# Optimization experiments

Measured on AMD Instinct MI355X. Metric: run time of the kernel, lower is better.

## Reference

```python
import jax, jax.numpy as jnp
import numpy as np

N = 4096
IN_F = 128
OUT_F = 64      # per-head out_features
HEADS = 4
ALPHA = 0.2     # LeakyReLU negative slope
NEG_FILL = -9e15


def setup_inputs() -> dict:
    key = jax.random.key(0)
    k_h, k_adj, k_W, k_a = jax.random.split(key, 4)
    h = jax.random.normal(k_h, (N, IN_F), dtype=jnp.float32)
    adj = jax.random.randint(k_adj, (N, N), 0, 2, dtype=jnp.int32)
    W = jax.random.normal(k_W, (IN_F, OUT_F * HEADS), dtype=jnp.float32) * 0.1
    a = jax.random.normal(k_a, (2 * OUT_F, 1), dtype=jnp.float32) * 0.1
    bias = jnp.zeros((OUT_F * HEADS,), dtype=jnp.float32)
    return {"h": h, "adj": adj, "W": W, "a": a, "bias": bias}


def reference(h, adj, W, a, bias):
    n = h.shape[0]
    Wh = (h @ W).reshape(n, HEADS, OUT_F)            # (N, H, F)
    # e_ij = leakyrelu(a_left . Wh_i + a_right . Wh_j)  (decomposed outer sum;
    # same math as concat([Wh_i, Wh_j]) @ a in the original)
    a_left = a[:OUT_F, 0]                            # (F,)
    a_right = a[OUT_F:, 0]                           # (F,)
    left = jnp.einsum('nhf,f->nh', Wh, a_left)       # (N, H)
    right = jnp.einsum('nhf,f->nh', Wh, a_right)     # (N, H)
    mask = adj > 0                                   # (N, N)
    outs = []
    for head in range(HEADS):                        # small fixed loop over heads
        e = left[:, head, None] + right[None, :, head]          # (N, N)
        e = jnp.where(e >= 0, e, ALPHA * e)                      # LeakyReLU
        e = jnp.where(mask, e, NEG_FILL)
        attn = jax.nn.softmax(e, axis=1)                         # (N, N)
        outs.append(attn @ Wh[:, head, :])                       # (N, F)
    out = jnp.concatenate(outs, axis=1)              # concat=True -> (N, H*F)
    return out + bias
```

## Files before the change

### kernel.cpp

```cpp
#include <hip/hip_runtime.h>
#include <hip/hip_bf16.h>

#define NN 4096
#define IN_F 128
#define OUT_F 64
#define C_TOT 256
#define ALPHA 0.2f
#define LOG2E 1.4426950408889634f

typedef float f32x4 __attribute__((ext_vector_type(4)));
typedef float f32x2 __attribute__((ext_vector_type(2)));
typedef __bf16 bf16x8 __attribute__((ext_vector_type(8)));

__device__ __forceinline__ unsigned fmap(float f) {
    unsigned u = __float_as_uint(f);
    return (u >> 31) ? ~u : (u | 0x80000000u);
}
__device__ __forceinline__ float funmap(unsigned u) {
    return (u >> 31) ? __uint_as_float(u & 0x7FFFFFFFu) : __uint_as_float(~u);
}
__device__ __forceinline__ unsigned short bfbits(float x) {
    union { __bf16 b; unsigned short u; } t;
    t.b = (__bf16)x;
    return t.u;
}
__device__ __forceinline__ void gl16(const void* g, void* l) {
    __builtin_amdgcn_global_load_lds((const __attribute__((address_space(1))) void*)g,
                                     (__attribute__((address_space(3))) void*)l, 16, 0, 0);
}

__global__ __launch_bounds__(256) void k_mask(
    const int* __restrict__ adj, unsigned* __restrict__ mask,
    const float* __restrict__ W, const float* __restrict__ a,
    unsigned short* __restrict__ WTbf, float* __restrict__ uLR,
    unsigned int* __restrict__ Rmax)
{
    const int tid = threadIdx.x;
    const int lane = tid & 63, wv = tid >> 6;
    const int row = blockIdx.x * 4 + wv;
    const int* __restrict__ ar = adj + (size_t)row * NN;
    unsigned* __restrict__ mr = mask + (size_t)row * 128;
    for (int c = 0; c < 8; ++c) {
        const int j0 = c * 512;
        unsigned w = 0u;
#pragma unroll
        for (int k = 0; k < 8; ++k) {
            const unsigned long long bb = __ballot(ar[j0 + k * 64 + lane] > 0);
            const unsigned lo = (unsigned)bb, hi = (unsigned)(bb >> 32);
            if ((lane >> 1) == k) w = (lane & 1) ? hi : lo;
        }
        if (lane < 16) {
            const int wi = c * 16 + lane;
            mr[(wi & 3) * 32 + (wi >> 2)] = w;
        }
    }

    if (blockIdx.x < 32) {
        const int b = blockIdx.x;
        const int c = b * 8 + (tid & 7);
#pragma unroll
        for (int pass = 0; pass < 4; ++pass) {
            const int k = pass * 32 + (tid >> 3);
            WTbf[(size_t)c * IN_F + k] = bfbits(W[k * C_TOT + c]);
        }
        if (b == 0) {
            if (tid < 4) Rmax[tid] = 0u;
            for (int o = tid; o < 1024; o += 256) {
                const int k = o >> 3, j = o & 7;
                const int hd = j & 3, side = j >> 2;
                float s = 0.f;
                for (int f = 0; f < OUT_F; ++f)
                    s = fmaf(W[k * C_TOT + hd * OUT_F + f], a[side * OUT_F + f], s);
                uLR[k * 8 + side * 4 + hd] = s;
            }
        }
    }
}

__global__ __launch_bounds__(256) void k_prep(
    const float* __restrict__ hmat, const unsigned short* __restrict__ WTbf,
    const float* __restrict__ uLR, unsigned short* __restrict__ WhT,
    float* __restrict__ leftT, float* __restrict__ rightT,
    unsigned int* __restrict__ Rmax)
{
    __shared__ float hs[16][132];
    __shared__ float us[128][8];
    const int tid = threadIdx.x;
    const int rowbase = blockIdx.x * 16;

    ((float4*)us)[tid] = ((const float4*)uLR)[tid];
#pragma unroll
    for (int p = 0; p < 8; ++p) {
        const int idx = p * 256 + tid;
        hs[idx >> 7][idx & 127] = hmat[(size_t)rowbase * IN_F + idx];
    }
    __syncthreads();

    const int lane = tid & 63, wv = tid >> 6;
    const int m16 = lane & 15, kg = lane >> 4;

    if (wv == 0) {
        const int row = lane >> 2, hd = lane & 3;
        float aL = 0.f, aR = 0.f;
#pragma unroll
        for (int k = 0; k < 128; k += 4) {
            const float4 hv = *(const float4*)&hs[row][k];
            aL = fmaf(hv.x, us[k][hd],   fmaf(hv.y, us[k+1][hd],   fmaf(hv.z, us[k+2][hd],   fmaf(hv.w, us[k+3][hd],   aL))));
            aR = fmaf(hv.x, us[k][hd+4], fmaf(hv.y, us[k+1][hd+4], fmaf(hv.z, us[k+2][hd+4], fmaf(hv.w, us[k+3][hd+4], aR))));
        }
        leftT [hd * NN + rowbase + row] = aL;
        rightT[hd * NN + rowbase + row] = aR * LOG2E;
        float mx = aR;
#pragma unroll
        for (int s = 4; s < 64; s <<= 1) mx = fmaxf(mx, __shfl_xor(mx, s, 64));
        if (lane < 4) atomicMax(&Rmax[hd], fmap(mx));
    }

    bf16x8 afr[4];
#pragma unroll
    for (int ks = 0; ks < 4; ++ks) {
        const float4 lo = *(const float4*)&hs[m16][ks * 32 + kg * 8];
        const float4 hi = *(const float4*)&hs[m16][ks * 32 + kg * 8 + 4];
        bf16x8 v;
        v[0] = (__bf16)lo.x; v[1] = (__bf16)lo.y; v[2] = (__bf16)lo.z; v[3] = (__bf16)lo.w;
        v[4] = (__bf16)hi.x; v[5] = (__bf16)hi.y; v[6] = (__bf16)hi.z; v[7] = (__bf16)hi.w;
        afr[ks] = v;
    }

#pragma unroll
    for (int nt0 = 0; nt0 < 4; ++nt0) {
        const int col = (wv * 4 + nt0) * 16 + m16;
        f32x4 acc = (f32x4){0.f, 0.f, 0.f, 0.f};
#pragma unroll
        for (int ks = 0; ks < 4; ++ks) {
            union { uint4 u; bf16x8 v; } B;
            B.u = *(const uint4*)(WTbf + (size_t)col * IN_F + ks * 32 + kg * 8);
            acc = __builtin_amdgcn_mfma_f32_16x16x32_bf16(afr[ks], B.v, acc, 0, 0, 0);
        }
#pragma unroll
        for (int i = 0; i < 4; ++i)
            WhT[(size_t)col * NN + rowbase + kg * 4 + i] = bfbits(acc[i]);
    }
}

__global__ __launch_bounds__(512, 8) void k_attn(
    const unsigned* __restrict__ mask,
    const unsigned short* __restrict__ WhT,
    const float* __restrict__ leftT,
    const float* __restrict__ rightT,
    const unsigned int* __restrict__ Rmax,
    float* __restrict__ out,
    float* __restrict__ num1,
    float* __restrict__ den)
{
    __shared__ unsigned short Bb[2][64 * 128];
    __shared__ float rlds[2048];

    const int tid = threadIdx.x;
    const int lane = tid & 63;
    const int wv = tid >> 6;
    const int rh = wv & 1;
    const int j4 = wv >> 1;
    const int jh = blockIdx.x & 1;
    const int hd = (blockIdx.x >> 1) & 3;
    const int rowbase = (blockIdx.x >> 3) * 32;
    const int m = lane & 15;
    const int kg = lane >> 4;
    const int sh = kg * 8;

    *(float4*)&rlds[tid * 4] =
        *(const float4*)(rightT + (size_t)hd * NN + jh * 2048 + tid * 4);
    unsigned mreg[16];
    {
        const unsigned* mrow = mask + (size_t)(rowbase + rh * 16 + m) * 128
                               + j4 * 32 + jh * 16;
#pragma unroll
        for (int p = 0; p < 4; ++p) {
            const uint4 v = *(const uint4*)(mrow + p * 4);
            mreg[p * 4 + 0] = v.x; mreg[p * 4 + 1] = v.y;
            mreg[p * 4 + 2] = v.z; mreg[p * 4 + 3] = v.w;
        }
    }

    const float lf = leftT[hd * NN + rowbase + rh * 16 + m];
    const float rmx = funmap(Rmax[hd]);
    const float x = lf + rmx;
    const float m0v = fmaxf(x, ALPHA * x);
    const float mp0 = m0v * LOG2E;
    const float lf2 = fmaf(lf, LOG2E, -mp0);
    const float qc = -0.8f * mp0;
    const f32x2 lf22 = (f32x2){lf2, lf2};
    const f32x2 al2  = (f32x2){ALPHA, ALPHA};
    const f32x2 qc2  = (f32x2){qc, qc};

    bf16x8 ONE8;
#pragma unroll
    for (int i = 0; i < 8; ++i) ONE8[i] = (__bf16)1.0f;

    const int srow0 = wv * 4 + (lane >> 4);
    const int g_lin = lane & 15;
    const int lg = g_lin ^ (srow0 & 15);
    const unsigned short* gsrc0 = WhT + (size_t)(hd * 64 + srow0) * NN
                                  + jh * 2048 + lg * 8;
    const unsigned short* gsrc1 = gsrc0 + (size_t)32 * NN;
    const int d0 = wv * 512 + lane * 8;

#define STAGE(buf, t) {                                  \
    gl16(gsrc0 + (t) * 128, &Bb[buf][d0]);               \
    gl16(gsrc1 + (t) * 128, &Bb[buf][4096 + d0]); }

    const int pg8 = ((j4 * 4 + kg) ^ m) * 8;
    const int bro = m * 128 + pg8;

    f32x4 acc0 = (f32x4){0,0,0,0}, acc1 = acc0, acc2 = acc0, acc3 = acc0;
    f32x4 accL = (f32x4){0,0,0,0};

    union F4 { f32x4 v; f32x2 h[2]; };

#define COMPUTE(buf, t) {                                                        \
    const unsigned aw = mreg[(t)] >> sh;                                         \
    F4 RA, RB;                                                                   \
    RA.v = *(const f32x4*)&rlds[(t) * 128 + j4 * 32 + sh];                       \
    RB.v = *(const f32x4*)&rlds[(t) * 128 + j4 * 32 + sh + 4];                   \
    const f32x2 rp2[4] = { RA.h[0], RA.h[1], RB.h[0], RB.h[1] };                 \
    union { __bf16 b[8]; bf16x8 v; } Af;                                         \
    _Pragma("unroll")                                                            \
    for (int e = 0; e < 4; ++e) {                                                \
        const f32x2 p = rp2[e] + lf22;                                           \
        const f32x2 q = __builtin_elementwise_fma(p, al2, qc2);                  \
        const float t0 = fmaxf(p.x, q.x), t1 = fmaxf(p.y, q.y);                  \
        float w0 = exp2f(t0), w1 = exp2f(t1);                                    \
        const unsigned mk0 = (unsigned)(((int)(aw << (31 - 2*e)))     >> 31);    \
        const unsigned mk1 = (unsigned)(((int)(aw << (31 - (2*e+1)))) >> 31);    \
        w0 = __uint_as_float(__float_as_uint(w0) & mk0);                         \
        w1 = __uint_as_float(__float_as_uint(w1) & mk1);                         \
        Af.b[2*e]   = (__bf16)w0;                                                \
        Af.b[2*e+1] = (__bf16)w1;                                                \
    }                                                                            \
    union { uint4 u; bf16x8 v; } B0, B1, B2, B3;                                 \
    B0.u = *(const uint4*)&Bb[buf][bro];                                         \
    B1.u = *(const uint4*)&Bb[buf][bro + 2048];                                  \
    B2.u = *(const uint4*)&Bb[buf][bro + 4096];                                  \
    B3.u = *(const uint4*)&Bb[buf][bro + 6144];                                  \
    acc0 = __builtin_amdgcn_mfma_f32_16x16x32_bf16(Af.v, B0.v, acc0, 0, 0, 0);   \
    acc1 = __builtin_amdgcn_mfma_f32_16x16x32_bf16(Af.v, B1.v, acc1, 0, 0, 0);   \
    acc2 = __builtin_amdgcn_mfma_f32_16x16x32_bf16(Af.v, B2.v, acc2, 0, 0, 0);   \
    acc3 = __builtin_amdgcn_mfma_f32_16x16x32_bf16(Af.v, B3.v, acc3, 0, 0, 0);   \
    accL = __builtin_amdgcn_mfma_f32_16x16x32_bf16(Af.v, ONE8, accL, 0, 0, 0);   \
}

    STAGE(0, 0);
    __syncthreads();

#pragma unroll
    for (int t = 0; t < 16; ++t) {
        if (t + 1 < 16) {
            STAGE((t + 1) & 1, t + 1);
            asm volatile("s_waitcnt vmcnt(2)" ::: "memory");
        } else {
            asm volatile("s_waitcnt vmcnt(0)" ::: "memory");
        }
        __builtin_amdgcn_sched_barrier(0);
        COMPUTE(t & 1, t);
        __builtin_amdgcn_sched_barrier(0);
        __builtin_amdgcn_s_barrier();
    }
#undef STAGE
#undef COMPUTE

    __syncthreads();
    float* comb = (float*)&Bb[0][0];
    if (j4 > 0) {
        float* c = comb + (((j4 - 1) * 2 + rh) * 64 + lane) * 20;
#pragma unroll
        for (int i = 0; i < 4; ++i) {
            c[ 0 + i] = acc0[i]; c[ 4 + i] = acc1[i];
            c[ 8 + i] = acc2[i]; c[12 + i] = acc3[i];
            c[16 + i] = accL[i];
        }
    }
    __syncthreads();
    if (j4 == 0) {
#pragma unroll
        for (int pt = 0; pt < 3; ++pt) {
            const float* c = comb + ((pt * 2 + rh) * 64 + lane) * 20;
#pragma unroll
            for (int i = 0; i < 4; ++i) {
                acc0[i] += c[ 0 + i]; acc1[i] += c[ 4 + i];
                acc2[i] += c[ 8 + i]; acc3[i] += c[12 + i];
                accL[i] += c[16 + i];
            }
        }
        float* numdst = jh ? num1 : out;
#pragma unroll
        for (int q = 0; q < 4; ++q) {
            const f32x4 A = (q == 0) ? acc0 : (q == 1) ? acc1 : (q == 2) ? acc2 : acc3;
            const int col = hd * 64 + q * 16 + m;
#pragma unroll
            for (int i = 0; i < 4; ++i) {
                const int r = kg * 4 + i;
                numdst[(size_t)(rowbase + rh * 16 + r) * C_TOT + col] = A[i];
            }
        }
        if (m == 0) {
#pragma unroll
            for (int i = 0; i < 4; ++i)
                den[(size_t)jh * 4 * NN + hd * NN + rowbase + rh * 16 + kg * 4 + i] = accL[i];
        }
    }
}

__global__ __launch_bounds__(256) void k_fin(
    float* __restrict__ out, const float* __restrict__ num1,
    const float* __restrict__ den, const float* __restrict__ bias)
{
    const int idx = blockIdx.x * 256 + threadIdx.x;
    const int row = idx >> 6;
    const int c4 = (idx & 63) * 4;
    const int hd = c4 >> 6;
    const float d = den[hd * NN + row] + den[4 * NN + hd * NN + row];
    const float rd = 1.0f / d;
    float4 n0 = *(float4*)(out + (size_t)row * C_TOT + c4);
    const float4 n1 = *(const float4*)(num1 + (size_t)row * C_TOT + c4);
    const float4 bv = *(const float4*)(bias + c4);
    n0.x = fmaf(n0.x + n1.x, rd, bv.x);
    n0.y = fmaf(n0.y + n1.y, rd, bv.y);
    n0.z = fmaf(n0.z + n1.z, rd, bv.z);
    n0.w = fmaf(n0.w + n1.w, rd, bv.w);
    *(float4*)(out + (size_t)row * C_TOT + c4) = n0;
}

extern "C" void kernel_launch(void* const* d_in, const int* in_sizes, int n_in,
                              void* d_out, int out_size, void* d_ws, size_t ws_size,
                              hipStream_t stream) {
    const float* hmat = (const float*)d_in[0];
    const int*   adj  = (const int*)d_in[1];
    const float* W    = (const float*)d_in[2];
    const float* a    = (const float*)d_in[3];
    const float* bias = (const float*)d_in[4];
    float* out = (float*)d_out;

    char* ws = (char*)d_ws;
    unsigned short* WhT  = (unsigned short*)(ws + 0x000000);
    float* rightT        = (float*)(ws + 0x280000);
    float* leftT         = (float*)(ws + 0x2A0000);
    unsigned short* WTbf = (unsigned short*)(ws + 0x2B0000);
    float* uLR           = (float*)(ws + 0x2C0000);
    unsigned int* Rmax   = (unsigned int*)(ws + 0x2C1000);
    unsigned* mask       = (unsigned*)(ws + 0x300000);
    float* num1          = (float*)(ws + 0x500000);
    float* den           = (float*)(ws + 0x900000);

    hipLaunchKernelGGL(k_mask, dim3(1024), dim3(256), 0, stream,
                       adj, mask, W, a, WTbf, uLR, Rmax);
    hipLaunchKernelGGL(k_prep, dim3(256),  dim3(256), 0, stream,
                       hmat, WTbf, uLR, WhT, leftT, rightT, Rmax);
    hipLaunchKernelGGL(k_attn, dim3(1024), dim3(512), 0, stream,
                       mask, WhT, leftT, rightT, Rmax, out, num1, den);
    hipLaunchKernelGGL(k_fin,  dim3(1024), dim3(256), 0, stream,
                       out, num1, den, bias);
}
```

Baseline: 71.34 us.

## Factor exp of leaky scores, enlarge attention blocks, deepen B staging pipeline

Rewrites the per-element weight exp2(max(p, alpha*p+c)) as max(exp(l)*exp(r), exp(alpha*l)*exp(alpha*r)). The exponentials of the right-hand terms are precomputed once per block in LDS and the per-row factors are computed once per thread, so the inner loop drops its transcendental ops in favour of multiplies. Blocks grow to 1024 threads covering 64 rows, which halves the grid and doubles reuse of each staged B tile. The B tile ring goes from 2 to 4 buffers with 3 tiles in flight, and the barrier now sits before the next stage. Risks are overflow or underflow in the factored products, higher LDS use, and lower occupancy at 1024 threads.

```diff
diff --git a/kernel.cpp b/kernel.cpp
--- a/kernel.cpp
+++ b/kernel.cpp
@@ -143,7 +143,7 @@
     }
 }
 
-__global__ __launch_bounds__(512, 8) void k_attn(
+__global__ __launch_bounds__(1024, 8) void k_attn(
     const unsigned* __restrict__ mask,
     const unsigned short* __restrict__ WhT,
     const float* __restrict__ leftT,
@@ -153,23 +153,41 @@
     float* __restrict__ num1,
     float* __restrict__ den)
 {
-    __shared__ unsigned short Bb[2][64 * 128];
-    __shared__ float rlds[2048];
+    __shared__ unsigned short Bb[4][64 * 128];
+    __shared__ float erl[2048];
+    __shared__ float er2l[2048];
 
     const int tid = threadIdx.x;
     const int lane = tid & 63;
-    const int wv = tid >> 6;
-    const int rh = wv & 1;
-    const int j4 = wv >> 1;
+    const int wvi = tid >> 6;
+    const int rh = wvi & 3;
+    const int j4 = wvi >> 2;
     const int jh = blockIdx.x & 1;
     const int hd = (blockIdx.x >> 1) & 3;
-    const int rowbase = (blockIdx.x >> 3) * 32;
+    const int rowbase = (blockIdx.x >> 3) * 64;
     const int m = lane & 15;
     const int kg = lane >> 4;
     const int sh = kg * 8;
 
-    *(float4*)&rlds[tid * 4] =
-        *(const float4*)(rightT + (size_t)hd * NN + jh * 2048 + tid * 4);
+    const int srow = tid >> 4;
+    const int g_lin = tid & 15;
+    const int lg = g_lin ^ (srow & 15);
+    const unsigned short* gsrc = WhT + (size_t)(hd * 64 + srow) * NN
+                                 + jh * 2048 + lg * 8;
+    const int d0 = srow * 128 + g_lin * 8;
+
+#define STAGE(buf, t) { gl16(gsrc + (t) * 128, &Bb[buf][d0]); }
+
+    STAGE(0, 0); STAGE(1, 1); STAGE(2, 2);
+
+    {
+        const float2 rv = *(const float2*)(rightT + (size_t)hd * NN + jh * 2048 + tid * 2);
+        erl [tid * 2    ] = exp2f(rv.x);
+        erl [tid * 2 + 1] = exp2f(rv.y);
+        er2l[tid * 2    ] = exp2f(ALPHA * rv.x);
+        er2l[tid * 2 + 1] = exp2f(ALPHA * rv.y);
+    }
+
     unsigned mreg[16];
     {
         const unsigned* mrow = mask + (size_t)(rowbase + rh * 16 + m) * 128
@@ -187,27 +205,16 @@
     const float x = lf + rmx;
     const float m0v = fmaxf(x, ALPHA * x);
     const float mp0 = m0v * LOG2E;
-    const float lf2 = fmaf(lf, LOG2E, -mp0);
-    const float qc = -0.8f * mp0;
-    const f32x2 lf22 = (f32x2){lf2, lf2};
-    const f32x2 al2  = (f32x2){ALPHA, ALPHA};
-    const f32x2 qc2  = (f32x2){qc, qc};
+    const float EL  = exp2f(fmaf(lf,         LOG2E, -mp0));
+    const float EL2 = exp2f(fmaf(lf * ALPHA, LOG2E, -mp0));
+    const f32x2 ELv  = (f32x2){EL,  EL};
+    const f32x2 EL2v = (f32x2){EL2, EL2};
 
     bf16x8 ONE8;
 #pragma unroll
     for (int i = 0; i < 8; ++i) ONE8[i] = (__bf16)1.0f;
 
-    const int srow0 = wv * 4 + (lane >> 4);
-    const int g_lin = lane & 15;
-    const int lg = g_lin ^ (srow0 & 15);
-    const unsigned short* gsrc0 = WhT + (size_t)(hd * 64 + srow0) * NN
-                                  + jh * 2048 + lg * 8;
-    const unsigned short* gsrc1 = gsrc0 + (size_t)32 * NN;
-    const int d0 = wv * 512 + lane * 8;
-
-#define STAGE(buf, t) {                                  \
-    gl16(gsrc0 + (t) * 128, &Bb[buf][d0]);               \
-    gl16(gsrc1 + (t) * 128, &Bb[buf][4096 + d0]); }
+    __syncthreads();
 
     const int pg8 = ((j4 * 4 + kg) ^ m) * 8;
     const int bro = m * 128 + pg8;
@@ -219,17 +226,20 @@
 
 #define COMPUTE(buf, t) {                                                        \
     const unsigned aw = mreg[(t)] >> sh;                                         \
-    F4 RA, RB;                                                                   \
-    RA.v = *(const f32x4*)&rlds[(t) * 128 + j4 * 32 + sh];                       \
-    RB.v = *(const f32x4*)&rlds[(t) * 128 + j4 * 32 + sh + 4];                   \
-    const f32x2 rp2[4] = { RA.h[0], RA.h[1], RB.h[0], RB.h[1] };                 \
+    F4 E0, E1, F0, F1;                                                           \
+    E0.v = *(const f32x4*)&erl [(t) * 128 + j4 * 32 + sh];                       \
+    E1.v = *(const f32x4*)&erl [(t) * 128 + j4 * 32 + sh + 4];                   \
+    F0.v = *(const f32x4*)&er2l[(t) * 128 + j4 * 32 + sh];                       \
+    F1.v = *(const f32x4*)&er2l[(t) * 128 + j4 * 32 + sh + 4];                   \
+    const f32x2 ep[4] = { E0.h[0], E0.h[1], E1.h[0], E1.h[1] };                  \
+    const f32x2 fp[4] = { F0.h[0], F0.h[1], F1.h[0], F1.h[1] };                  \
     union { __bf16 b[8]; bf16x8 v; } Af;                                         \
     _Pragma("unroll")                                                            \
     for (int e = 0; e < 4; ++e) {                                                \
-        const f32x2 p = rp2[e] + lf22;                                           \
-        const f32x2 q = __builtin_elementwise_fma(p, al2, qc2);                  \
-        const float t0 = fmaxf(p.x, q.x), t1 = fmaxf(p.y, q.y);                  \
-        float w0 = exp2f(t0), w1 = exp2f(t1);                                    \
+        const f32x2 full = ep[e] * ELv;                        \
+        const f32x2 leak = fp[e] * EL2v;                       \
+        float w0 = fmaxf(full.x, leak.x);                     \
+        float w1 = fmaxf(full.y, leak.y);                                        \
         const unsigned mk0 = (unsigned)(((int)(aw << (31 - 2*e)))     >> 31);    \
         const unsigned mk1 = (unsigned)(((int)(aw << (31 - (2*e+1)))) >> 31);    \
         w0 = __uint_as_float(__float_as_uint(w0) & mk0);                         \
@@ -249,21 +259,16 @@
     accL = __builtin_amdgcn_mfma_f32_16x16x32_bf16(Af.v, ONE8, accL, 0, 0, 0);   \
 }
 
-    STAGE(0, 0);
-    __syncthreads();
-
 #pragma unroll
     for (int t = 0; t < 16; ++t) {
-        if (t + 1 < 16) {
-            STAGE((t + 1) & 1, t + 1);
-            asm volatile("s_waitcnt vmcnt(2)" ::: "memory");
-        } else {
-            asm volatile("s_waitcnt vmcnt(0)" ::: "memory");
-        }
-        __builtin_amdgcn_sched_barrier(0);
-        COMPUTE(t & 1, t);
+        if (t <= 13)      { asm volatile("s_waitcnt vmcnt(2)" ::: "memory"); }
+        else if (t == 14) { asm volatile("s_waitcnt vmcnt(1)" ::: "memory"); }
+        else              { asm volatile("s_waitcnt vmcnt(0)" ::: "memory"); }
         __builtin_amdgcn_sched_barrier(0);
         __builtin_amdgcn_s_barrier();
+        if (t + 3 < 16) STAGE((t + 3) & 3, t + 3);
+        COMPUTE(t & 3, t);
+        __builtin_amdgcn_sched_barrier(0);
     }
 #undef STAGE
 #undef COMPUTE
@@ -271,7 +276,7 @@
     __syncthreads();
     float* comb = (float*)&Bb[0][0];
     if (j4 > 0) {
-        float* c = comb + (((j4 - 1) * 2 + rh) * 64 + lane) * 20;
+        float* c = comb + (((j4 - 1) * 4 + rh) * 64 + lane) * 20;
 #pragma unroll
         for (int i = 0; i < 4; ++i) {
             c[ 0 + i] = acc0[i]; c[ 4 + i] = acc1[i];
@@ -283,7 +288,7 @@
     if (j4 == 0) {
 #pragma unroll
         for (int pt = 0; pt < 3; ++pt) {
-            const float* c = comb + ((pt * 2 + rh) * 64 + lane) * 20;
+            const float* c = comb + ((pt * 4 + rh) * 64 + lane) * 20;
 #pragma unroll
             for (int i = 0; i < 4; ++i) {
                 acc0[i] += c[ 0 + i]; acc1[i] += c[ 4 + i];
@@ -355,7 +360,7 @@
                        adj, mask, W, a, WTbf, uLR, Rmax);
     hipLaunchKernelGGL(k_prep, dim3(256),  dim3(256), 0, stream,
                        hmat, WTbf, uLR, WhT, leftT, rightT, Rmax);
-    hipLaunchKernelGGL(k_attn, dim3(1024), dim3(512), 0, stream,
+    hipLaunchKernelGGL(k_attn, dim3(512),  dim3(1024), 0, stream,
                        mask, WhT, leftT, rightT, Rmax, out, num1, den);
     hipLaunchKernelGGL(k_fin,  dim3(1024), dim3(256), 0, stream,
                        out, num1, den, bias);
```

After: 64.00 us. -10.3%, faster.
